# Performance work log

Measured on AMD Instinct MI355X. Metric: run time of the kernel, lower is better.

Reference implementation:

```python
import jax, jax.numpy as jnp
import numpy as np

N = 8192
IN_F = 512
OUT_F = 256
EDGE_P = 0.02  # adjacency density


def setup_inputs() -> dict:
    key = jax.random.key(0)
    k1, k2, k3, k4 = jax.random.split(key, 4)
    x = jax.random.normal(k1, (N, IN_F), dtype=jnp.float32)
    # xavier_uniform with gain=1.414 ~ std gain*sqrt(2/(fan_in+fan_out))
    W = jax.random.normal(k2, (IN_F, OUT_F), dtype=jnp.float32) * (1.414 * np.sqrt(2.0 / (IN_F + OUT_F)))
    a = jax.random.normal(k3, (2 * OUT_F, 1), dtype=jnp.float32) * (1.414 * np.sqrt(2.0 / (2 * OUT_F + 1)))
    adj = (jax.random.uniform(k4, (N, N)) < EDGE_P).astype(jnp.float32)
    return {"x": x, "adj": adj, "W": W, "a": a}


def reference(x, adj, W, a):
    h = x @ W                        # [N, F]
    F = h.shape[1]
    # repeat/cat reduces to an outer sum of two [N] vectors.
    s_src = (h @ a[:F]).squeeze(-1)  # [N], contribution of h_i
    s_dst = (h @ a[F:]).squeeze(-1)  # [N], contribution of h_j
    e = jax.nn.leaky_relu(s_src[:, None] + s_dst[None, :], negative_slope=0.2)  # [N, N]
    # NOTE: original code softmaxes over the FULL row, THEN multiplies by adj.
    attention = jax.nn.softmax(e, axis=1) * adj  # [N, N]
    h_prime = attention @ h                      # [N, F]
    return h_prime, attention
```

## Files before the change

### kernel.cpp

```cpp
#include <hip/hip_runtime.h>
#include <hip/hip_bf16.h>

#define N_NODES 8192
#define IN_F    512
#define OUT_F   256
#define MAXNZ   512

typedef float v4f  __attribute__((ext_vector_type(4)));
typedef __attribute__((ext_vector_type(8)))  short bf16x8;
typedef __attribute__((ext_vector_type(16))) float f32x16;
typedef unsigned short u16;
typedef unsigned int   u32;

__device__ __forceinline__ u16 f2bf(float f) {
  u32 u = __float_as_uint(f);
  u += 0x7fffu + ((u >> 16) & 1u);
  return (u16)(u >> 16);
}
__device__ __forceinline__ float bf2f(u16 h) {
  return __uint_as_float(((u32)h) << 16);
}

__global__ __launch_bounds__(256) void k_cast_x(const float* __restrict__ x,
                                                u16* __restrict__ x_hi,
                                                u16* __restrict__ x_lo) {
  const int idx = blockIdx.x * 256 + threadIdx.x;
  const float4 v = ((const float4*)x)[idx];
  u16 h0 = f2bf(v.x), h1 = f2bf(v.y), h2 = f2bf(v.z), h3 = f2bf(v.w);
  u16 l0 = f2bf(v.x - bf2f(h0)), l1 = f2bf(v.y - bf2f(h1));
  u16 l2 = f2bf(v.z - bf2f(h2)), l3 = f2bf(v.w - bf2f(h3));
  uint2 hp, lp;
  hp.x = (u32)h0 | ((u32)h1 << 16); hp.y = (u32)h2 | ((u32)h3 << 16);
  lp.x = (u32)l0 | ((u32)l1 << 16); lp.y = (u32)l2 | ((u32)l3 << 16);
  ((uint2*)x_hi)[idx] = hp;
  ((uint2*)x_lo)[idx] = lp;
}

__global__ __launch_bounds__(256) void k_cast_wt(const float* __restrict__ W,
                                                 u16* __restrict__ wt_hi,
                                                 u16* __restrict__ wt_lo) {
  const int k = blockIdx.x;
  const int n = threadIdx.x;
  const float v = W[(size_t)k * OUT_F + n];
  const u16 h = f2bf(v);
  wt_hi[(size_t)n * IN_F + k] = h;
  wt_lo[(size_t)n * IN_F + k] = f2bf(v - bf2f(h));
}

__global__ __launch_bounds__(256) void k_gemm_mfma(const u16* __restrict__ x_hi,
                                                   const u16* __restrict__ x_lo,
                                                   const u16* __restrict__ wt_hi,
                                                   const u16* __restrict__ wt_lo,
                                                   float* __restrict__ h,
                                                   u16* __restrict__ h_bf) {
  __shared__ u16 As_hi[64 * 40], As_lo[64 * 40], Bs_hi[64 * 40], Bs_lo[64 * 40];
  const int t    = threadIdx.x;
  const int bn   = blockIdx.x & 3;
  const int bm   = blockIdx.x >> 2;
  const int m0   = bm * 64, n0 = bn * 64;
  const int lane = t & 63;
  const int w    = t >> 6;
  const int wm   = w & 1, wn = w >> 1;

  const int sm = t >> 2;
  const int sk = (t & 3) * 8;

  f32x16 acc = {};

  for (int k0 = 0; k0 < IN_F; k0 += 32) {
    *(bf16x8*)&As_hi[sm * 40 + sk] = *(const bf16x8*)&x_hi[(size_t)(m0 + sm) * IN_F + k0 + sk];
    *(bf16x8*)&As_lo[sm * 40 + sk] = *(const bf16x8*)&x_lo[(size_t)(m0 + sm) * IN_F + k0 + sk];
    *(bf16x8*)&Bs_hi[sm * 40 + sk] = *(const bf16x8*)&wt_hi[(size_t)(n0 + sm) * IN_F + k0 + sk];
    *(bf16x8*)&Bs_lo[sm * 40 + sk] = *(const bf16x8*)&wt_lo[(size_t)(n0 + sm) * IN_F + k0 + sk];
    __syncthreads();
    const int am = wm * 32 + (lane & 31);
    const int bn_ = wn * 32 + (lane & 31);
#pragma unroll
    for (int kk = 0; kk < 2; ++kk) {
      const int ko = kk * 16 + (lane >> 5) * 8;
      const bf16x8 ah = *(const bf16x8*)&As_hi[am * 40 + ko];
      const bf16x8 al = *(const bf16x8*)&As_lo[am * 40 + ko];
      const bf16x8 bh = *(const bf16x8*)&Bs_hi[bn_ * 40 + ko];
      const bf16x8 bl = *(const bf16x8*)&Bs_lo[bn_ * 40 + ko];
      acc = __builtin_amdgcn_mfma_f32_32x32x16_bf16(ah, bh, acc, 0, 0, 0);
      acc = __builtin_amdgcn_mfma_f32_32x32x16_bf16(al, bh, acc, 0, 0, 0);
      acc = __builtin_amdgcn_mfma_f32_32x32x16_bf16(ah, bl, acc, 0, 0, 0);
    }
    __syncthreads();
  }
  const int col = n0 + wn * 32 + (lane & 31);
#pragma unroll
  for (int r = 0; r < 16; ++r) {
    const int row = m0 + wm * 32 + (r & 3) + 8 * (r >> 2) + 4 * (lane >> 5);
    const float v = acc[r];
    h[(size_t)row * OUT_F + col]    = v;
    h_bf[(size_t)row * OUT_F + col] = f2bf(v);
  }
}

__global__ __launch_bounds__(256) void k_scores(const float* __restrict__ h,
                                                const float* __restrict__ a,
                                                float* __restrict__ s_src,
                                                float* __restrict__ s_dst) {
  const int row = blockIdx.x * 4 + (threadIdx.x >> 6);
  const int l   = threadIdx.x & 63;
  const float4 hv = ((const float4*)(h + (size_t)row * OUT_F))[l];
  const float4 a0 = ((const float4*)a)[l];
  const float4 a1 = ((const float4*)(a + OUT_F))[l];
  float p0 = hv.x * a0.x + hv.y * a0.y + hv.z * a0.z + hv.w * a0.w;
  float p1 = hv.x * a1.x + hv.y * a1.y + hv.z * a1.z + hv.w * a1.w;
#pragma unroll
  for (int off = 32; off > 0; off >>= 1) {
    p0 += __shfl_down(p0, off);
    p1 += __shfl_down(p1, off);
  }
  if (l == 0) { s_src[row] = p0; s_dst[row] = p1; }
}

__device__ __forceinline__ float lrelu_exp(float v) {
  const float e = v > 0.f ? v : 0.2f * v;
  return __expf(e);
}

__global__ __launch_bounds__(256) void k_attn(const float* __restrict__ adj,
                                              const u16* __restrict__ h_bf,
                                              const float* __restrict__ s_src,
                                              const float* __restrict__ s_dst,
                                              float* __restrict__ out_hp,
                                              float* __restrict__ out_att) {
  __shared__ float nza[MAXNZ];
  __shared__ int   nzj[MAXNZ];
  __shared__ float redbuf[4];
  __shared__ int   cnt;

  const int t = threadIdx.x;
  const int i = blockIdx.x;
  const float ssrc = s_src[i];
  if (t == 0) cnt = 0;

  const float4* sd4 = (const float4*)s_dst;
  float4 sd[8];
#pragma unroll
  for (int c = 0; c < 8; ++c) sd[c] = sd4[c * 256 + t];

  float lsum = 0.f;
#pragma unroll
  for (int c = 0; c < 8; ++c) {
    lsum += lrelu_exp(ssrc + sd[c].x) + lrelu_exp(ssrc + sd[c].y)
          + lrelu_exp(ssrc + sd[c].z) + lrelu_exp(ssrc + sd[c].w);
  }
#pragma unroll
  for (int off = 32; off > 0; off >>= 1) lsum += __shfl_down(lsum, off);
  if ((t & 63) == 0) redbuf[t >> 6] = lsum;
  __syncthreads();
  const float inv = 1.0f / (redbuf[0] + redbuf[1] + redbuf[2] + redbuf[3]);

  const v4f* adj4 = (const v4f*)(adj + (size_t)i * N_NODES);
  v4f*       att4 = (v4f*)(out_att + (size_t)i * N_NODES);
  v4f av[8];
#pragma unroll
  for (int c = 0; c < 8; ++c) av[c] = __builtin_nontemporal_load(adj4 + c * 256 + t);
#pragma unroll
  for (int c = 0; c < 8; ++c) {
    v4f att;
    att.x = av[c].x * (lrelu_exp(ssrc + sd[c].x) * inv);
    att.y = av[c].y * (lrelu_exp(ssrc + sd[c].y) * inv);
    att.z = av[c].z * (lrelu_exp(ssrc + sd[c].z) * inv);
    att.w = av[c].w * (lrelu_exp(ssrc + sd[c].w) * inv);
    __builtin_nontemporal_store(att, att4 + c * 256 + t);
    const int j = (c * 256 + t) * 4;
    if (av[c].x != 0.f) { const int k = atomicAdd(&cnt, 1); if (k < MAXNZ) { nzj[k] = j + 0; nza[k] = att.x; } }
    if (av[c].y != 0.f) { const int k = atomicAdd(&cnt, 1); if (k < MAXNZ) { nzj[k] = j + 1; nza[k] = att.y; } }
    if (av[c].z != 0.f) { const int k = atomicAdd(&cnt, 1); if (k < MAXNZ) { nzj[k] = j + 2; nza[k] = att.z; } }
    if (av[c].w != 0.f) { const int k = atomicAdd(&cnt, 1); if (k < MAXNZ) { nzj[k] = j + 3; nza[k] = att.w; } }
  }
  __syncthreads();

  const int n = cnt < MAXNZ ? cnt : MAXNZ;
  float acc = 0.f;
#pragma unroll 8
  for (int k = 0; k < n; ++k) {
    acc = fmaf(nza[k], bf2f(h_bf[(size_t)nzj[k] * OUT_F + t]), acc);
  }
  out_hp[(size_t)i * OUT_F + t] = acc;
}

extern "C" void kernel_launch(void* const* d_in, const int* in_sizes, int n_in,
                              void* d_out, int out_size, void* d_ws, size_t ws_size,
                              hipStream_t stream) {
  const float* x   = (const float*)d_in[0];
  const float* adj = (const float*)d_in[1];
  const float* W   = (const float*)d_in[2];
  const float* a   = (const float*)d_in[3];

  float* out_hp  = (float*)d_out;
  float* out_att = (float*)d_out + (size_t)N_NODES * OUT_F;

  char* ws = (char*)d_ws;
  float* h_ws    = (float*)ws;                       ws += (size_t)N_NODES * OUT_F * 4;
  float* ssrc_ws = (float*)ws;                       ws += N_NODES * 4;
  float* sdst_ws = (float*)ws;                       ws += N_NODES * 4;
  u16*   x_hi    = (u16*)ws;                         ws += (size_t)N_NODES * IN_F * 2;
  u16*   x_lo    = (u16*)ws;                         ws += (size_t)N_NODES * IN_F * 2;
  u16*   wt_hi   = (u16*)ws;                         ws += (size_t)OUT_F * IN_F * 2;
  u16*   wt_lo   = (u16*)ws;                         ws += (size_t)OUT_F * IN_F * 2;
  u16*   h_bf    = (u16*)ws;                         ws += (size_t)N_NODES * OUT_F * 2;

  k_cast_x<<<(N_NODES * IN_F / 4) / 256, 256, 0, stream>>>(x, x_hi, x_lo);
  k_cast_wt<<<IN_F, OUT_F, 0, stream>>>(W, wt_hi, wt_lo);
  k_gemm_mfma<<<(N_NODES / 64) * (OUT_F / 64), 256, 0, stream>>>(x_hi, x_lo, wt_hi, wt_lo, h_ws, h_bf);
  k_scores<<<N_NODES / 4, 256, 0, stream>>>(h_ws, a, ssrc_ws, sdst_ws);
  k_attn<<<N_NODES, 256, 0, stream>>>(adj, h_bf, ssrc_ws, sdst_ws, out_hp, out_att);
}
```

Measured before the change: 509.9 us.

## Fuse score projection into GEMM epilogue and widen GEMM K-tile

The separate scores kernel and the fp32 h buffer are removed. The GEMM epilogue now takes dot products with both halves of a, reduces them across the 32-lane column group with xor shuffles, and atomically accumulates into zeroed s_src/s_dst buffers, which requires a memset. The GEMM K-tile grows from 32 to 64 to halve the number of barriers. The attention kernel now caches the exp values in registers instead of recomputing them. The atomics make the summation order nondeterministic and add contention of four column blocks per row.

New measurement: 508.1 us. No clear change (-0.3%).

```diff
diff --git a/kernel.cpp b/kernel.cpp
--- a/kernel.cpp
+++ b/kernel.cpp
@@ -47,13 +47,16 @@
   wt_lo[(size_t)n * IN_F + k] = f2bf(v - bf2f(h));
 }
 
+#define GBK 64
 __global__ __launch_bounds__(256) void k_gemm_mfma(const u16* __restrict__ x_hi,
                                                    const u16* __restrict__ x_lo,
                                                    const u16* __restrict__ wt_hi,
                                                    const u16* __restrict__ wt_lo,
-                                                   float* __restrict__ h,
-                                                   u16* __restrict__ h_bf) {
-  __shared__ u16 As_hi[64 * 40], As_lo[64 * 40], Bs_hi[64 * 40], Bs_lo[64 * 40];
+                                                   const float* __restrict__ a,
+                                                   u16* __restrict__ h_bf,
+                                                   float* __restrict__ s_src,
+                                                   float* __restrict__ s_dst) {
+  __shared__ u16 As_hi[64 * 68], As_lo[64 * 68], Bs_hi[64 * 68], Bs_lo[64 * 68];
   const int t    = threadIdx.x;
   const int bn   = blockIdx.x & 3;
   const int bm   = blockIdx.x >> 2;
@@ -63,58 +66,54 @@
   const int wm   = w & 1, wn = w >> 1;
 
   const int sm = t >> 2;
-  const int sk = (t & 3) * 8;
+  const int sk = (t & 3) * 16;
 
   f32x16 acc = {};
 
-  for (int k0 = 0; k0 < IN_F; k0 += 32) {
-    *(bf16x8*)&As_hi[sm * 40 + sk] = *(const bf16x8*)&x_hi[(size_t)(m0 + sm) * IN_F + k0 + sk];
-    *(bf16x8*)&As_lo[sm * 40 + sk] = *(const bf16x8*)&x_lo[(size_t)(m0 + sm) * IN_F + k0 + sk];
-    *(bf16x8*)&Bs_hi[sm * 40 + sk] = *(const bf16x8*)&wt_hi[(size_t)(n0 + sm) * IN_F + k0 + sk];
-    *(bf16x8*)&Bs_lo[sm * 40 + sk] = *(const bf16x8*)&wt_lo[(size_t)(n0 + sm) * IN_F + k0 + sk];
+  for (int k0 = 0; k0 < IN_F; k0 += GBK) {
+#pragma unroll
+    for (int i = 0; i < 2; ++i) {
+      const int ko = sk + i * 8;
+      *(bf16x8*)&As_hi[sm * 68 + ko] = *(const bf16x8*)&x_hi[(size_t)(m0 + sm) * IN_F + k0 + ko];
+      *(bf16x8*)&As_lo[sm * 68 + ko] = *(const bf16x8*)&x_lo[(size_t)(m0 + sm) * IN_F + k0 + ko];
+      *(bf16x8*)&Bs_hi[sm * 68 + ko] = *(const bf16x8*)&wt_hi[(size_t)(n0 + sm) * IN_F + k0 + ko];
+      *(bf16x8*)&Bs_lo[sm * 68 + ko] = *(const bf16x8*)&wt_lo[(size_t)(n0 + sm) * IN_F + k0 + ko];
+    }
     __syncthreads();
-    const int am = wm * 32 + (lane & 31);
+    const int am  = wm * 32 + (lane & 31);
     const int bn_ = wn * 32 + (lane & 31);
 #pragma unroll
-    for (int kk = 0; kk < 2; ++kk) {
+    for (int kk = 0; kk < 4; ++kk) {
       const int ko = kk * 16 + (lane >> 5) * 8;
-      const bf16x8 ah = *(const bf16x8*)&As_hi[am * 40 + ko];
-      const bf16x8 al = *(const bf16x8*)&As_lo[am * 40 + ko];
-      const bf16x8 bh = *(const bf16x8*)&Bs_hi[bn_ * 40 + ko];
-      const bf16x8 bl = *(const bf16x8*)&Bs_lo[bn_ * 40 + ko];
+      const bf16x8 ah = *(const bf16x8*)&As_hi[am * 68 + ko];
+      const bf16x8 al = *(const bf16x8*)&As_lo[am * 68 + ko];
+      const bf16x8 bh = *(const bf16x8*)&Bs_hi[bn_ * 68 + ko];
+      const bf16x8 bl = *(const bf16x8*)&Bs_lo[bn_ * 68 + ko];
       acc = __builtin_amdgcn_mfma_f32_32x32x16_bf16(ah, bh, acc, 0, 0, 0);
       acc = __builtin_amdgcn_mfma_f32_32x32x16_bf16(al, bh, acc, 0, 0, 0);
       acc = __builtin_amdgcn_mfma_f32_32x32x16_bf16(ah, bl, acc, 0, 0, 0);
     }
     __syncthreads();
   }
-  const int col = n0 + wn * 32 + (lane & 31);
+  const int colg = n0 + wn * 32 + (lane & 31);
+  const float asv = a[colg];
+  const float adv = a[OUT_F + colg];
 #pragma unroll
   for (int r = 0; r < 16; ++r) {
     const int row = m0 + wm * 32 + (r & 3) + 8 * (r >> 2) + 4 * (lane >> 5);
     const float v = acc[r];
-    h[(size_t)row * OUT_F + col]    = v;
-    h_bf[(size_t)row * OUT_F + col] = f2bf(v);
-  }
-}
-
-__global__ __launch_bounds__(256) void k_scores(const float* __restrict__ h,
-                                                const float* __restrict__ a,
-                                                float* __restrict__ s_src,
-                                                float* __restrict__ s_dst) {
-  const int row = blockIdx.x * 4 + (threadIdx.x >> 6);
-  const int l   = threadIdx.x & 63;
-  const float4 hv = ((const float4*)(h + (size_t)row * OUT_F))[l];
-  const float4 a0 = ((const float4*)a)[l];
-  const float4 a1 = ((const float4*)(a + OUT_F))[l];
-  float p0 = hv.x * a0.x + hv.y * a0.y + hv.z * a0.z + hv.w * a0.w;
-  float p1 = hv.x * a1.x + hv.y * a1.y + hv.z * a1.z + hv.w * a1.w;
-#pragma unroll
-  for (int off = 32; off > 0; off >>= 1) {
-    p0 += __shfl_down(p0, off);
-    p1 += __shfl_down(p1, off);
-  }
-  if (l == 0) { s_src[row] = p0; s_dst[row] = p1; }
+    h_bf[(size_t)row * OUT_F + colg] = f2bf(v);
+    float vs = v * asv, vd = v * adv;
+#pragma unroll
+    for (int off = 1; off < 32; off <<= 1) {
+      vs += __shfl_xor(vs, off);
+      vd += __shfl_xor(vd, off);
+    }
+    if ((lane & 31) == 0) {
+      atomicAdd(&s_src[row], vs);
+      atomicAdd(&s_dst[row], vd);
+    }
+  }
 }
 
 __device__ __forceinline__ float lrelu_exp(float v) {
@@ -139,15 +138,16 @@
   if (t == 0) cnt = 0;
 
   const float4* sd4 = (const float4*)s_dst;
-  float4 sd[8];
-#pragma unroll
-  for (int c = 0; c < 8; ++c) sd[c] = sd4[c * 256 + t];
-
+  float4 p[8];
   float lsum = 0.f;
 #pragma unroll
   for (int c = 0; c < 8; ++c) {
-    lsum += lrelu_exp(ssrc + sd[c].x) + lrelu_exp(ssrc + sd[c].y)
-          + lrelu_exp(ssrc + sd[c].z) + lrelu_exp(ssrc + sd[c].w);
+    const float4 s = sd4[c * 256 + t];
+    p[c].x = lrelu_exp(ssrc + s.x);
+    p[c].y = lrelu_exp(ssrc + s.y);
+    p[c].z = lrelu_exp(ssrc + s.z);
+    p[c].w = lrelu_exp(ssrc + s.w);
+    lsum += p[c].x + p[c].y + p[c].z + p[c].w;
   }
 #pragma unroll
   for (int off = 32; off > 0; off >>= 1) lsum += __shfl_down(lsum, off);
@@ -163,10 +163,10 @@
 #pragma unroll
   for (int c = 0; c < 8; ++c) {
     v4f att;
-    att.x = av[c].x * (lrelu_exp(ssrc + sd[c].x) * inv);
-    att.y = av[c].y * (lrelu_exp(ssrc + sd[c].y) * inv);
-    att.z = av[c].z * (lrelu_exp(ssrc + sd[c].z) * inv);
-    att.w = av[c].w * (lrelu_exp(ssrc + sd[c].w) * inv);
+    att.x = av[c].x * (p[c].x * inv);
+    att.y = av[c].y * (p[c].y * inv);
+    att.z = av[c].z * (p[c].z * inv);
+    att.w = av[c].w * (p[c].w * inv);
     __builtin_nontemporal_store(att, att4 + c * 256 + t);
     const int j = (c * 256 + t) * 4;
     if (av[c].x != 0.f) { const int k = atomicAdd(&cnt, 1); if (k < MAXNZ) { nzj[k] = j + 0; nza[k] = att.x; } }
@@ -197,7 +197,6 @@
   float* out_att = (float*)d_out + (size_t)N_NODES * OUT_F;
 
   char* ws = (char*)d_ws;
-  float* h_ws    = (float*)ws;                       ws += (size_t)N_NODES * OUT_F * 4;
   float* ssrc_ws = (float*)ws;                       ws += N_NODES * 4;
   float* sdst_ws = (float*)ws;                       ws += N_NODES * 4;
   u16*   x_hi    = (u16*)ws;                         ws += (size_t)N_NODES * IN_F * 2;
@@ -206,9 +205,11 @@
   u16*   wt_lo   = (u16*)ws;                         ws += (size_t)OUT_F * IN_F * 2;
   u16*   h_bf    = (u16*)ws;                         ws += (size_t)N_NODES * OUT_F * 2;
 
+  hipMemsetAsync(ssrc_ws, 0, 2 * N_NODES * sizeof(float), stream);
+
   k_cast_x<<<(N_NODES * IN_F / 4) / 256, 256, 0, stream>>>(x, x_hi, x_lo);
   k_cast_wt<<<IN_F, OUT_F, 0, stream>>>(W, wt_hi, wt_lo);
-  k_gemm_mfma<<<(N_NODES / 64) * (OUT_F / 64), 256, 0, stream>>>(x_hi, x_lo, wt_hi, wt_lo, h_ws, h_bf);
-  k_scores<<<N_NODES / 4, 256, 0, stream>>>(h_ws, a, ssrc_ws, sdst_ws);
+  k_gemm_mfma<<<(N_NODES / 64) * (OUT_F / 64), 256, 0, stream>>>(
+      x_hi, x_lo, wt_hi, wt_lo, a, h_bf, ssrc_ws, sdst_ws);
   k_attn<<<N_NODES, 256, 0, stream>>>(adj, h_bf, ssrc_ws, sdst_ws, out_hp, out_att);
 }
```
